# Kernel optimization log

Measured on AMD Instinct MI355X. Metric: run time of the kernel, lower is better.

## Reference

```python
import jax, jax.numpy as jnp
import numpy as np

N, M, D, DV = 8192, 8192, 64, 64

def setup_inputs() -> dict:
    key = jax.random.key(0)
    kq, kk, kv = jax.random.split(key, 3)
    Q = jax.random.normal(kq, (N, D), dtype=jnp.float32)
    K = jax.random.normal(kk, (M, D), dtype=jnp.float32)
    V = jax.random.normal(kv, (M, DV), dtype=jnp.float32)
    return {"Q": Q, "K": K, "V": V}

def reference(Q, K, V):
    d = K.shape[-1]
    scores = jnp.einsum('nd,md->nm', Q, K) / jnp.sqrt(jnp.float32(d))  # [N, M]
    attn = jax.nn.softmax(scores, axis=-1)
    return attn @ V  # [N, DV]
```

## Files before the change

kernel.cpp:

```cpp
#include <hip/hip_runtime.h>


#define NQ 8192
#define NK 8192

typedef float f32x4 __attribute__((ext_vector_type(4)));
typedef short short8 __attribute__((ext_vector_type(8)));
union U4 { uint4 u; short8 s; };

#define MFMA16 __builtin_amdgcn_mfma_f32_16x16x32_bf16

__device__ __forceinline__ unsigned pk2(float a, float b) {
    unsigned ua = __builtin_bit_cast(unsigned, a);
    unsigned ub = __builtin_bit_cast(unsigned, b);
    ua = (ua + 0x7FFFu + ((ua >> 16) & 1u)) >> 16;
    ub = (ub + 0x7FFFu + ((ub >> 16) & 1u)) & 0xFFFF0000u;
    return ua | ub;
}

__global__ __launch_bounds__(256)
void prepass(const float* __restrict__ Kg, const float* __restrict__ Vg,
             uint4* __restrict__ Kb4, uint4* __restrict__ Vt4) {
    __shared__ float ld[64 * 33];
    const int t = threadIdx.x, b = blockIdx.x;

    {
        const int kl = t >> 3, dg = t & 7;
        const int e = kl & 1, i16 = kl >> 1, h = dg >> 2, q = dg & 3;
        const float* gp = Kg + (size_t)(b * 32 + kl) * 64 + dg * 8;
        float4 f0 = *(const float4*)gp;
        float4 f1 = *(const float4*)(gp + 4);
        uint4 o = make_uint4(pk2(f0.x, f0.y), pk2(f0.z, f0.w),
                             pk2(f1.x, f1.y), pk2(f1.z, f1.w));
        Kb4[(size_t)(b * 4 + e * 2 + h) * 64 + i16 * 4 + q] = o;
    }
    {
        const int key = t >> 3, dg = t & 7;
        const float* gp = Vg + (size_t)(b * 32 + key) * 64 + dg * 8;
        float4 f0 = *(const float4*)gp;
        float4 f1 = *(const float4*)(gp + 4);
        ld[(dg * 8 + 0) * 33 + key] = f0.x;
        ld[(dg * 8 + 1) * 33 + key] = f0.y;
        ld[(dg * 8 + 2) * 33 + key] = f0.z;
        ld[(dg * 8 + 3) * 33 + key] = f0.w;
        ld[(dg * 8 + 4) * 33 + key] = f1.x;
        ld[(dg * 8 + 5) * 33 + key] = f1.y;
        ld[(dg * 8 + 6) * 33 + key] = f1.z;
        ld[(dg * 8 + 7) * 33 + key] = f1.w;
    }
    __syncthreads();
    {
        const int dim = t >> 2, kq = t & 3;
        const int dt = dim >> 4, i16 = dim & 15;
        float v[8];
        #pragma unroll
        for (int j = 0; j < 8; ++j) v[j] = ld[dim * 33 + kq * 8 + j];
        uint4 o = make_uint4(pk2(v[0], v[1]), pk2(v[2], v[3]),
                             pk2(v[4], v[5]), pk2(v[6], v[7]));
        Vt4[(size_t)(b * 4 + dt) * 64 + i16 * 4 + kq] = o;
    }
}

__global__ __launch_bounds__(1024, 4)
void attn_main(const float* __restrict__ Qg,
               const uint4* __restrict__ Kb4,
               const uint4* __restrict__ Vt4,
               float* __restrict__ Og) {
    __shared__ uint4 shb4[4160];
    float* sF = (float*)shb4;
    unsigned* shu = (unsigned*)shb4;

    const int t = threadIdx.x, w = t >> 6, lane = t & 63;
    const int q = lane >> 4, i16 = lane & 15;
    const int qb0 = blockIdx.x * 32;
    const int lsl = i16 * 4 + q;

    const float SCL = 0.18033688011112042f;
    short8 aq0, aq1, aq2, aq3;
    {
        const float* qp0 = Qg + (size_t)(qb0 + i16) * 64 + q * 8;
        const float* qp1 = Qg + (size_t)(qb0 + 16 + i16) * 64 + q * 8;
        U4 u;
        float4 f0, f1;
        f0 = *(const float4*)(qp0);      f1 = *(const float4*)(qp0 + 4);
        u.u = make_uint4(pk2(f0.x * SCL, f0.y * SCL), pk2(f0.z * SCL, f0.w * SCL),
                         pk2(f1.x * SCL, f1.y * SCL), pk2(f1.z * SCL, f1.w * SCL));
        aq0 = u.s;
        f0 = *(const float4*)(qp0 + 32); f1 = *(const float4*)(qp0 + 36);
        u.u = make_uint4(pk2(f0.x * SCL, f0.y * SCL), pk2(f0.z * SCL, f0.w * SCL),
                         pk2(f1.x * SCL, f1.y * SCL), pk2(f1.z * SCL, f1.w * SCL));
        aq1 = u.s;
        f0 = *(const float4*)(qp1);      f1 = *(const float4*)(qp1 + 4);
        u.u = make_uint4(pk2(f0.x * SCL, f0.y * SCL), pk2(f0.z * SCL, f0.w * SCL),
                         pk2(f1.x * SCL, f1.y * SCL), pk2(f1.z * SCL, f1.w * SCL));
        aq2 = u.s;
        f0 = *(const float4*)(qp1 + 32); f1 = *(const float4*)(qp1 + 36);
        u.u = make_uint4(pk2(f0.x * SCL, f0.y * SCL), pk2(f0.z * SCL, f0.w * SCL),
                         pk2(f1.x * SCL, f1.y * SCL), pk2(f1.z * SCL, f1.w * SCL));
        aq3 = u.s;
    }
    short8 bones;
    { U4 u; u.u = make_uint4(0x3F803F80u, 0x3F803F80u, 0x3F803F80u, 0x3F803F80u); bones = u.s; }

    f32x4 acc[2][4];
    f32x4 lacc[2];
    #pragma unroll
    for (int rt = 0; rt < 2; ++rt) {
        #pragma unroll
        for (int dt = 0; dt < 4; ++dt) { acc[rt][dt][0]=0.f; acc[rt][dt][1]=0.f; acc[rt][dt][2]=0.f; acc[rt][dt][3]=0.f; }
        lacc[rt][0]=0.f; lacc[rt][1]=0.f; lacc[rt][2]=0.f; lacc[rt][3]=0.f;
    }

    const int tpw = ((i16 >> 2) & 1) + 2 * q + 32 * (i16 >> 3);
    const int pp  = i16 & 3;
    const int tpr = (q & 1) + 2 * ((i16 >> 2) & 3) + 8 * (i16 & 3) + 32 * (q >> 1);

    uint4 kf0[4], vf0[4], kf1[4], vf1[4];

#define LOAD_TILE(TT, KD, VD)                                                        \
    do {                                                                             \
        const size_t cb = ((size_t)(TT) * 16 + w) * 4;                               \
        _Pragma("unroll")                                                            \
        for (int eh = 0; eh < 4; ++eh)                                               \
            (KD)[eh] = Kb4[(cb + eh) * 64 + lsl];                                    \
        _Pragma("unroll")                                                            \
        for (int dt = 0; dt < 4; ++dt)                                               \
            (VD)[dt] = Vt4[(cb + dt) * 64 + lsl];                                    \
    } while (0)

#define COMPUTE(KD, VD)                                                              \
    do {                                                                             \
        f32x4 sfr[2][2];                                                             \
        _Pragma("unroll")                                                            \
        for (int rt = 0; rt < 2; ++rt)                                               \
            _Pragma("unroll")                                                        \
            for (int e = 0; e < 2; ++e) {                                            \
                f32x4 sacc;                                                          \
                sacc[0]=-16.f; sacc[1]=-16.f; sacc[2]=-16.f; sacc[3]=-16.f;          \
                U4 u0; u0.u = (KD)[e * 2 + 0];                                       \
                U4 u1; u1.u = (KD)[e * 2 + 1];                                       \
                sacc = MFMA16(rt ? aq2 : aq0, u0.s, sacc, 0, 0, 0);                  \
                sacc = MFMA16(rt ? aq3 : aq1, u1.s, sacc, 0, 0, 0);                  \
                sfr[rt][e] = sacc;                                                   \
            }                                                                        \
        _Pragma("unroll")                                                            \
        for (int rt = 0; rt < 2; ++rt) {                                             \
            const int rbase = (w * 2 + rt) * 256;                                    \
            _Pragma("unroll")                                                        \
            for (int r = 0; r < 4; ++r) {                                            \
                float p0 = __builtin_amdgcn_exp2f(sfr[rt][0][r]);                    \
                float p1 = __builtin_amdgcn_exp2f(sfr[rt][1][r]);                    \
                shu[rbase + (tpw + 8 * r) * 4 + pp] = pk2(p0, p1);                   \
            }                                                                        \
        }                                                                            \
        U4 ap0, ap1;                                                                 \
        ap0.u = shb4[(w * 2 + 0) * 64 + tpr];                                        \
        ap1.u = shb4[(w * 2 + 1) * 64 + tpr];                                        \
        lacc[0] = MFMA16(ap0.s, bones, lacc[0], 0, 0, 0);                            \
        lacc[1] = MFMA16(ap1.s, bones, lacc[1], 0, 0, 0);                            \
        _Pragma("unroll")                                                            \
        for (int dt = 0; dt < 4; ++dt) {                                             \
            U4 bv; bv.u = (VD)[dt];                                                  \
            acc[0][dt] = MFMA16(ap0.s, bv.s, acc[0][dt], 0, 0, 0);                   \
            acc[1][dt] = MFMA16(ap1.s, bv.s, acc[1][dt], 0, 0, 0);                   \
        }                                                                            \
    } while (0)

    LOAD_TILE(0, kf0, vf0);
    #pragma unroll 1
    for (int tt = 0; tt < 16; tt += 2) {
        LOAD_TILE(tt + 1, kf1, vf1);
        COMPUTE(kf0, vf0);
        LOAD_TILE((tt + 2) & 15, kf0, vf0);
        COMPUTE(kf1, vf1);
    }

    __syncthreads();
    for (int step = 8; step >= 1; step >>= 1) {
        if (w >= step && w < 2 * step) {
            float* base = sF + (w - step) * 2080;
            #pragma unroll
            for (int rt = 0; rt < 2; ++rt) {
                #pragma unroll
                for (int dt = 0; dt < 4; ++dt)
                    #pragma unroll
                    for (int r = 0; r < 4; ++r)
                        base[(rt * 16 + 4 * q + r) * 64 + dt * 16 + i16] = acc[rt][dt][r];
                if (i16 == 0) {
                    #pragma unroll
                    for (int r = 0; r < 4; ++r) base[2048 + rt * 16 + 4 * q + r] = lacc[rt][r];
                }
            }
        }
        __syncthreads();
        if (w < step) {
            const float* base = sF + w * 2080;
            #pragma unroll
            for (int rt = 0; rt < 2; ++rt) {
                #pragma unroll
                for (int dt = 0; dt < 4; ++dt)
                    #pragma unroll
                    for (int r = 0; r < 4; ++r)
                        acc[rt][dt][r] += base[(rt * 16 + 4 * q + r) * 64 + dt * 16 + i16];
                #pragma unroll
                for (int r = 0; r < 4; ++r) lacc[rt][r] += base[2048 + rt * 16 + 4 * q + r];
            }
        }
        __syncthreads();
    }

    if (w == 0) {
        #pragma unroll
        for (int rt = 0; rt < 2; ++rt)
            #pragma unroll
            for (int r = 0; r < 4; ++r) {
                const float inv = 1.0f / lacc[rt][r];
                #pragma unroll
                for (int dt = 0; dt < 4; ++dt)
                    sF[(rt * 16 + 4 * q + r) * 64 + dt * 16 + i16] = acc[rt][dt][r] * inv;
            }
    }
    __syncthreads();
    if (t < 512) {
        const int row = t >> 4, ds = t & 15;
        float4 o = *(const float4*)(sF + row * 64 + ds * 4);
        *(float4*)(Og + (size_t)(qb0 + row) * 64 + ds * 4) = o;
    }
}

extern "C" void kernel_launch(void* const* d_in, const int* in_sizes, int n_in,
                              void* d_out, int out_size, void* d_ws, size_t ws_size,
                              hipStream_t stream) {
    const float* Q = (const float*)d_in[0];
    const float* K = (const float*)d_in[1];
    const float* V = (const float*)d_in[2];
    float* O = (float*)d_out;
    uint4* Kb4 = (uint4*)d_ws;
    uint4* Vt4 = (uint4*)((char*)d_ws + (1 << 20));
    hipLaunchKernelGGL(prepass, dim3(256), dim3(256), 0, stream, K, V, Kb4, Vt4);
    hipLaunchKernelGGL(attn_main, dim3(NQ / 32), dim3(1024), 0, stream, Q, Kb4, Vt4, O);
}
```

Baseline: 99.11 us.

## Split K/V loads, stagger tile order per block, and sum softmax denominators in fp32

Splits the tile load into separate K and V loads so V is fetched after the PV MFMAs, and places scheduling barriers that pin the load/compute interleave. Each block starts its key-tile sweep at an offset given by its block index, spreading L2 accesses across tiles. The row-sum MFMA against a ones vector is replaced by fp32 scalar accumulation of the exp values, followed by a cross-lane shuffle reduction. The launch bound is expressed as waves_per_eu(4,4). Risks are more VALU work for the sums, a denominator now summed from unrounded fp32 probabilities while the numerator uses bf16-rounded ones, and stalls caused by the fixed schedule.

```diff
diff --git a/kernel.cpp b/kernel.cpp
--- a/kernel.cpp
+++ b/kernel.cpp
@@ -61,7 +61,8 @@
     }
 }
 
-__global__ __launch_bounds__(1024, 4)
+__global__ __launch_bounds__(1024)
+__attribute__((amdgpu_waves_per_eu(4, 4)))
 void attn_main(const float* __restrict__ Qg,
                const uint4* __restrict__ Kb4,
                const uint4* __restrict__ Vt4,
@@ -74,6 +75,7 @@
     const int q = lane >> 4, i16 = lane & 15;
     const int qb0 = blockIdx.x * 32;
     const int lsl = i16 * 4 + q;
+    const int phase = blockIdx.x & 15;
 
     const float SCL = 0.18033688011112042f;
     short8 aq0, aq1, aq2, aq3;
@@ -99,81 +101,105 @@
                          pk2(f1.x * SCL, f1.y * SCL), pk2(f1.z * SCL, f1.w * SCL));
         aq3 = u.s;
     }
-    short8 bones;
-    { U4 u; u.u = make_uint4(0x3F803F80u, 0x3F803F80u, 0x3F803F80u, 0x3F803F80u); bones = u.s; }
 
     f32x4 acc[2][4];
-    f32x4 lacc[2];
+    float lsum[2][4];
     #pragma unroll
     for (int rt = 0; rt < 2; ++rt) {
         #pragma unroll
         for (int dt = 0; dt < 4; ++dt) { acc[rt][dt][0]=0.f; acc[rt][dt][1]=0.f; acc[rt][dt][2]=0.f; acc[rt][dt][3]=0.f; }
-        lacc[rt][0]=0.f; lacc[rt][1]=0.f; lacc[rt][2]=0.f; lacc[rt][3]=0.f;
+        #pragma unroll
+        for (int r = 0; r < 4; ++r) lsum[rt][r] = 0.f;
     }
 
     const int tpw = ((i16 >> 2) & 1) + 2 * q + 32 * (i16 >> 3);
     const int pp  = i16 & 3;
     const int tpr = (q & 1) + 2 * ((i16 >> 2) & 3) + 8 * (i16 & 3) + 32 * (q >> 1);
 
-    uint4 kf0[4], vf0[4], kf1[4], vf1[4];
-
-#define LOAD_TILE(TT, KD, VD)                                                        \
-    do {                                                                             \
-        const size_t cb = ((size_t)(TT) * 16 + w) * 4;                               \
+    uint4 kfA[4], kfB[4], vf[4];
+    U4 ap0, ap1;
+
+#define LOAD_K(TT, KD)                                                               \
+    do {                                                                             \
+        const int cb = ((((TT) + phase) & 15) * 16 + w) * 4;                         \
         _Pragma("unroll")                                                            \
         for (int eh = 0; eh < 4; ++eh)                                               \
-            (KD)[eh] = Kb4[(cb + eh) * 64 + lsl];                                    \
+            (KD)[eh] = Kb4[(size_t)(cb + eh) * 64 + lsl];                            \
+    } while (0)
+
+#define LOAD_V(TT)                                                                   \
+    do {                                                                             \
+        const int cb = ((((TT) + phase) & 15) * 16 + w) * 4;                         \
         _Pragma("unroll")                                                            \
         for (int dt = 0; dt < 4; ++dt)                                               \
-            (VD)[dt] = Vt4[(cb + dt) * 64 + lsl];                                    \
-    } while (0)
-
-#define COMPUTE(KD, VD)                                                              \
-    do {                                                                             \
-        f32x4 sfr[2][2];                                                             \
-        _Pragma("unroll")                                                            \
-        for (int rt = 0; rt < 2; ++rt)                                               \
-            _Pragma("unroll")                                                        \
-            for (int e = 0; e < 2; ++e) {                                            \
-                f32x4 sacc;                                                          \
-                sacc[0]=-16.f; sacc[1]=-16.f; sacc[2]=-16.f; sacc[3]=-16.f;          \
-                U4 u0; u0.u = (KD)[e * 2 + 0];                                       \
-                U4 u1; u1.u = (KD)[e * 2 + 1];                                       \
-                sacc = MFMA16(rt ? aq2 : aq0, u0.s, sacc, 0, 0, 0);                  \
-                sacc = MFMA16(rt ? aq3 : aq1, u1.s, sacc, 0, 0, 0);                  \
-                sfr[rt][e] = sacc;                                                   \
-            }                                                                        \
+            vf[dt] = Vt4[(size_t)(cb + dt) * 64 + lsl];                              \
+    } while (0)
+
+#define QKEXP(KD)                                                                    \
+    do {                                                                             \
         _Pragma("unroll")                                                            \
         for (int rt = 0; rt < 2; ++rt) {                                             \
+            f32x4 s0, s1;                                                            \
+            s0[0]=-16.f; s0[1]=-16.f; s0[2]=-16.f; s0[3]=-16.f;                      \
+            s1[0]=-16.f; s1[1]=-16.f; s1[2]=-16.f; s1[3]=-16.f;                      \
+            U4 u0, u1, u2, u3;                                                       \
+            u0.u = (KD)[0]; u1.u = (KD)[1]; u2.u = (KD)[2]; u3.u = (KD)[3];          \
+            s0 = MFMA16(rt ? aq2 : aq0, u0.s, s0, 0, 0, 0);                          \
+            s0 = MFMA16(rt ? aq3 : aq1, u1.s, s0, 0, 0, 0);                          \
+            s1 = MFMA16(rt ? aq2 : aq0, u2.s, s1, 0, 0, 0);                          \
+            s1 = MFMA16(rt ? aq3 : aq1, u3.s, s1, 0, 0, 0);                          \
             const int rbase = (w * 2 + rt) * 256;                                    \
             _Pragma("unroll")                                                        \
             for (int r = 0; r < 4; ++r) {                                            \
-                float p0 = __builtin_amdgcn_exp2f(sfr[rt][0][r]);                    \
-                float p1 = __builtin_amdgcn_exp2f(sfr[rt][1][r]);                    \
+                float p0 = __builtin_amdgcn_exp2f(s0[r]);                            \
+                float p1 = __builtin_amdgcn_exp2f(s1[r]);                            \
+                lsum[rt][r] += p0;                                                   \
+                lsum[rt][r] += p1;                                                   \
                 shu[rbase + (tpw + 8 * r) * 4 + pp] = pk2(p0, p1);                   \
             }                                                                        \
         }                                                                            \
-        U4 ap0, ap1;                                                                 \
         ap0.u = shb4[(w * 2 + 0) * 64 + tpr];                                        \
         ap1.u = shb4[(w * 2 + 1) * 64 + tpr];                                        \
-        lacc[0] = MFMA16(ap0.s, bones, lacc[0], 0, 0, 0);                            \
-        lacc[1] = MFMA16(ap1.s, bones, lacc[1], 0, 0, 0);                            \
+    } while (0)
+
+#define PV()                                                                         \
+    do {                                                                             \
         _Pragma("unroll")                                                            \
         for (int dt = 0; dt < 4; ++dt) {                                             \
-            U4 bv; bv.u = (VD)[dt];                                                  \
+            U4 bv; bv.u = vf[dt];                                                    \
             acc[0][dt] = MFMA16(ap0.s, bv.s, acc[0][dt], 0, 0, 0);                   \
             acc[1][dt] = MFMA16(ap1.s, bv.s, acc[1][dt], 0, 0, 0);                   \
         }                                                                            \
     } while (0)
 
-    LOAD_TILE(0, kf0, vf0);
+    LOAD_K(0, kfA);
+    LOAD_V(0);
     #pragma unroll 1
     for (int tt = 0; tt < 16; tt += 2) {
-        LOAD_TILE(tt + 1, kf1, vf1);
-        COMPUTE(kf0, vf0);
-        LOAD_TILE((tt + 2) & 15, kf0, vf0);
-        COMPUTE(kf1, vf1);
-    }
+        LOAD_K(tt + 1, kfB);
+        __builtin_amdgcn_sched_barrier(0);
+        QKEXP(kfA);
+        PV();
+        LOAD_V(tt + 1);
+        LOAD_K(tt + 2, kfA);
+        __builtin_amdgcn_sched_barrier(0);
+        QKEXP(kfB);
+        PV();
+        LOAD_V(tt + 2);
+        __builtin_amdgcn_sched_barrier(0);
+    }
+
+    #pragma unroll
+    for (int rt = 0; rt < 2; ++rt)
+        #pragma unroll
+        for (int r = 0; r < 4; ++r) {
+            float v = lsum[rt][r];
+            v += __shfl_xor(v, 1);
+            v += __shfl_xor(v, 2);
+            v += __shfl_xor(v, 4);
+            v += __shfl_xor(v, 8);
+            lsum[rt][r] = v;
+        }
 
     __syncthreads();
     for (int step = 8; step >= 1; step >>= 1) {
@@ -188,7 +214,7 @@
                         base[(rt * 16 + 4 * q + r) * 64 + dt * 16 + i16] = acc[rt][dt][r];
                 if (i16 == 0) {
                     #pragma unroll
-                    for (int r = 0; r < 4; ++r) base[2048 + rt * 16 + 4 * q + r] = lacc[rt][r];
+                    for (int r = 0; r < 4; ++r) base[2048 + rt * 16 + 4 * q + r] = lsum[rt][r];
                 }
             }
         }
@@ -203,7 +229,7 @@
                     for (int r = 0; r < 4; ++r)
                         acc[rt][dt][r] += base[(rt * 16 + 4 * q + r) * 64 + dt * 16 + i16];
                 #pragma unroll
-                for (int r = 0; r < 4; ++r) lacc[rt][r] += base[2048 + rt * 16 + 4 * q + r];
+                for (int r = 0; r < 4; ++r) lsum[rt][r] += base[2048 + rt * 16 + 4 * q + r];
             }
         }
         __syncthreads();
@@ -214,7 +240,7 @@
         for (int rt = 0; rt < 2; ++rt)
             #pragma unroll
             for (int r = 0; r < 4; ++r) {
-                const float inv = 1.0f / lacc[rt][r];
+                const float inv = 1.0f / lsum[rt][r];
                 #pragma unroll
                 for (int dt = 0; dt < 4; ++dt)
                     sF[(rt * 16 + 4 * q + r) * 64 + dt * 16 + i16] = acc[rt][dt][r] * inv;
```

Result: slower. 127.0 us (+28.2%).
